# Performance work log

Hardware: AMD Instinct MI355X
Metric: run time of the kernel (lower is better)

Reference implementation:

```python
import math
import jax, jax.numpy as jnp
import numpy as np

PH, PW = 16, 16
MAPPER_X = [0, 0, 6, 0, 0, 1, 1, 4, 5, 1, 3, 0, 0, 0, 3, 2]
MAPPER_Y = [0, 1, 0, 5, 2, 0, 2, 0, 0, 6, 0, 4, 6, 3, 5, 2]


def _make_dct_bases(ph, pw, mapper_x, mapper_y):
    bases = []
    for u, v in zip(mapper_x, mapper_y):
        Bu = np.cos(np.pi * (np.arange(ph) + 0.5) * u / ph) / math.sqrt(ph)
        if u != 0:
            Bu = Bu * math.sqrt(2)
        Bv = np.cos(np.pi * (np.arange(pw) + 0.5) * v / pw) / math.sqrt(pw)
        if v != 0:
            Bv = Bv * math.sqrt(2)
        bases.append(np.outer(Bu, Bv))
    return jnp.asarray(np.stack(bases, axis=0), dtype=jnp.float32)  # [M, ph, pw]


def setup_inputs() -> dict:
    key = jax.random.key(0)
    x = jax.random.normal(key, (16, 64, 224, 224), dtype=jnp.float32)
    dct_bases = _make_dct_bases(PH, PW, MAPPER_X, MAPPER_Y)
    return {"x": x, "dct_bases": dct_bases}


def reference(x, dct_bases):
    # x: [B, C, H, W]; dct_bases: [M, ph, pw]
    B, C, H, W = x.shape
    M, ph, pw = dct_bases.shape
    # H, W chosen divisible by ph, pw -> pad_h = pad_w = 0 (faithful to the no-pad path)
    Hp, Wp = H // ph, W // pw
    x_mean = x.mean(axis=1)                              # [B, H, W]
    patches = x_mean.reshape(B, Hp, ph, Wp, pw)          # non-overlapping unfold
    coeff = jnp.einsum('bhiwj,mij->bmhw', patches, dct_bases)  # [B, M, Hp, Wp]
    # nearest upsample by (ph, pw): broadcast each coeff over its patch footprint
    freq = jnp.broadcast_to(coeff[:, :, :, None, :, None], (B, M, Hp, ph, Wp, pw))
    return freq.reshape(B, M, H, W)
```

## Files before the change

kernel.cpp:

```cpp
#include <hip/hip_runtime.h>

#define B_   16
#define C_   64
#define H_   224
#define W_   224
#define M_   16
#define PH   16
#define PW   16
#define HP   14
#define WP   14
#define PLANE (H_ * W_)
#define PLANE4 (PLANE / 4)
#define NCOEF (B_ * M_ * HP * WP)

__global__ __launch_bounds__(256)
void k1_mean(const float* __restrict__ x, float* __restrict__ mean) {
    const int f4 = blockIdx.x * 256 + threadIdx.x;
    const int b  = blockIdx.y;
    const float4* p = (const float4*)x + (size_t)b * C_ * PLANE4 + f4;
    float4 acc = {0.f, 0.f, 0.f, 0.f};
#pragma unroll 16
    for (int c = 0; c < C_; ++c) {
        float4 v = p[(size_t)c * PLANE4];
        acc.x += v.x; acc.y += v.y; acc.z += v.z; acc.w += v.w;
    }
    const float inv = 1.f / (float)C_;
    acc.x *= inv; acc.y *= inv; acc.z *= inv; acc.w *= inv;
    ((float4*)mean)[(size_t)b * PLANE4 + f4] = acc;
}

__global__ __launch_bounds__(256)
void k2a_coeff(const float* __restrict__ mean, const float* __restrict__ bases,
               float* __restrict__ coeff) {
    const int pid = blockIdx.x;
    const int wp  = pid % WP;
    const int hp  = pid / WP;
    const int b   = blockIdx.y;

    __shared__ float patch[PH * 20];

    const int t = threadIdx.x;
    if (t < 64) {
        const int i  = t >> 2;
        const int c4 = t & 3;
        const float4 v = *(const float4*)(mean + (size_t)b * PLANE
                                          + (size_t)(hp * PH + i) * W_
                                          + wp * PW + c4 * 4);
        *(float4*)&patch[i * 20 + c4 * 4] = v;
    }
    __syncthreads();

    const int m = t >> 4;
    const int s = t & 15;
    const float* brow = bases + m * (PH * PW) + s * PW;
    float partial = 0.f;
#pragma unroll
    for (int k = 0; k < 16; ++k)
        partial += patch[s * 20 + k] * brow[k];
    partial += __shfl_xor(partial, 1);
    partial += __shfl_xor(partial, 2);
    partial += __shfl_xor(partial, 4);
    partial += __shfl_xor(partial, 8);
    if (s == 0)
        coeff[(((size_t)b * M_ + m) * HP + hp) * WP + wp] = partial;
}

__global__ __launch_bounds__(256)
void k2b_broadcast(const float* __restrict__ coeff, float* __restrict__ out) {
    const int o4 = blockIdx.x * 256 + threadIdx.x;
    const int bm = blockIdx.y;
    const int w4 = o4 % (W_ / 4);
    const int h  = o4 / (W_ / 4);
    const int hp = h >> 4;
    const int wp = w4 >> 2;
    const float c = coeff[((size_t)bm * HP + hp) * WP + wp];
    float4 v = {c, c, c, c};
    ((float4*)out)[(size_t)bm * PLANE4 + o4] = v;
}

extern "C" void kernel_launch(void* const* d_in, const int* in_sizes, int n_in,
                              void* d_out, int out_size, void* d_ws, size_t ws_size,
                              hipStream_t stream) {
    const float* x     = (const float*)d_in[0];
    const float* bases = (const float*)d_in[1];
    float* out         = (float*)d_out;

    float* mean  = (float*)d_ws;
    float* coeff = mean + (size_t)B_ * PLANE;

    dim3 g1(PLANE4 / 256, B_);
    k1_mean<<<g1, 256, 0, stream>>>(x, mean);

    dim3 g2(HP * WP, B_);
    k2a_coeff<<<g2, 256, 0, stream>>>(mean, bases, coeff);

    dim3 g3(PLANE4 / 256, B_ * M_);
    k2b_broadcast<<<g3, 256, 0, stream>>>(coeff, out);
}
```

Before: 304.2 us.

## Fuse DCT coefficient computation with upsampled broadcast write

```diff
diff --git a/kernel.cpp b/kernel.cpp
--- a/kernel.cpp
+++ b/kernel.cpp
@@ -11,7 +11,9 @@
 #define WP   14
 #define PLANE (H_ * W_)
 #define PLANE4 (PLANE / 4)
-#define NCOEF (B_ * M_ * HP * WP)
+#define BAND  (PH * W_)
+#define BAND4 (BAND / 4)
+#define LSTRIDE 228
 
 __global__ __launch_bounds__(256)
 void k1_mean(const float* __restrict__ x, float* __restrict__ mean) {
@@ -30,52 +32,51 @@
 }
 
 __global__ __launch_bounds__(256)
-void k2a_coeff(const float* __restrict__ mean, const float* __restrict__ bases,
-               float* __restrict__ coeff) {
-    const int pid = blockIdx.x;
-    const int wp  = pid % WP;
-    const int hp  = pid / WP;
-    const int b   = blockIdx.y;
+void k2_dct_write(const float* __restrict__ mean, const float* __restrict__ bases,
+                  float* __restrict__ out) {
+    const int m  = blockIdx.x;
+    const int hp = blockIdx.y;
+    const int b  = blockIdx.z;
+    const int t  = threadIdx.x;
 
-    __shared__ float patch[PH * 20];
+    __shared__ float band[PH * LSTRIDE];
+    __shared__ float cf[WP];
 
-    const int t = threadIdx.x;
-    if (t < 64) {
-        const int i  = t >> 2;
-        const int c4 = t & 3;
-        const float4 v = *(const float4*)(mean + (size_t)b * PLANE
-                                          + (size_t)(hp * PH + i) * W_
-                                          + wp * PW + c4 * 4);
-        *(float4*)&patch[i * 20 + c4 * 4] = v;
+    const float4* src = (const float4*)(mean + (size_t)b * PLANE + (size_t)hp * BAND);
+    for (int j = t; j < BAND4; j += 256) {
+        const int row  = j / (W_ / 4);
+        const int col4 = j % (W_ / 4);
+        *(float4*)&band[row * LSTRIDE + col4 * 4] = src[j];
     }
     __syncthreads();
 
-    const int m = t >> 4;
-    const int s = t & 15;
-    const float* brow = bases + m * (PH * PW) + s * PW;
-    float partial = 0.f;
+    if (t < WP * 16) {
+        const int wp = t >> 4;
+        const int s  = t & 15;
+        const float* brow = bases + m * (PH * PW) + s * PW;
+        float partial = 0.f;
 #pragma unroll
-    for (int k = 0; k < 16; ++k)
-        partial += patch[s * 20 + k] * brow[k];
-    partial += __shfl_xor(partial, 1);
-    partial += __shfl_xor(partial, 2);
-    partial += __shfl_xor(partial, 4);
-    partial += __shfl_xor(partial, 8);
-    if (s == 0)
-        coeff[(((size_t)b * M_ + m) * HP + hp) * WP + wp] = partial;
-}
+        for (int k = 0; k < 16; ++k)
+            partial += band[s * LSTRIDE + wp * PW + k] * brow[k];
+        partial += __shfl_xor(partial, 1);
+        partial += __shfl_xor(partial, 2);
+        partial += __shfl_xor(partial, 4);
+        partial += __shfl_xor(partial, 8);
+        if (s == 0) cf[wp] = partial;
+    }
+    __syncthreads();
 
-__global__ __launch_bounds__(256)
-void k2b_broadcast(const float* __restrict__ coeff, float* __restrict__ out) {
-    const int o4 = blockIdx.x * 256 + threadIdx.x;
-    const int bm = blockIdx.y;
-    const int w4 = o4 % (W_ / 4);
-    const int h  = o4 / (W_ / 4);
-    const int hp = h >> 4;
-    const int wp = w4 >> 2;
-    const float c = coeff[((size_t)bm * HP + hp) * WP + wp];
-    float4 v = {c, c, c, c};
-    ((float4*)out)[(size_t)bm * PLANE4 + o4] = v;
+    float4* dst = (float4*)(out + ((size_t)b * M_ + m) * PLANE + (size_t)hp * BAND);
+#pragma unroll
+    for (int j4 = 0; j4 < BAND4; j4 += 256) {
+        const int j    = j4 + t;
+        const int col4 = j % (W_ / 4);
+        if (j < BAND4) {
+            const float c = cf[col4 >> 2];
+            float4 v = {c, c, c, c};
+            dst[j] = v;
+        }
+    }
 }
 
 extern "C" void kernel_launch(void* const* d_in, const int* in_sizes, int n_in,
@@ -85,15 +86,11 @@
     const float* bases = (const float*)d_in[1];
     float* out         = (float*)d_out;
 
-    float* mean  = (float*)d_ws;
-    float* coeff = mean + (size_t)B_ * PLANE;
+    float* mean = (float*)d_ws;
 
     dim3 g1(PLANE4 / 256, B_);
     k1_mean<<<g1, 256, 0, stream>>>(x, mean);
 
-    dim3 g2(HP * WP, B_);
-    k2a_coeff<<<g2, 256, 0, stream>>>(mean, bases, coeff);
-
-    dim3 g3(PLANE4 / 256, B_ * M_);
-    k2b_broadcast<<<g3, 256, 0, stream>>>(coeff, out);
+    dim3 g2(M_, HP, B_);
+    k2_dct_write<<<g2, 256, 0, stream>>>(mean, bases, out);
 }
```

New measurement: 302.4 us. No clear change (-0.6%).
